# Kernel tuning notes

Hardware: AMD Instinct MI355X
Metric: run time of the kernel (lower is better)

The kernel has to match this reference:

```python
import jax, jax.numpy as jnp
import numpy as np

B, FIN, H, W = 16, 256, 32, 32
NH, FH = 8, 64
CIN = FIN + 2  # fin + 2 coordinate-grid pos channels
COUT = NH * FH


def setup_inputs() -> dict:
    key = jax.random.key(0)
    ks = jax.random.split(key, 9)
    s = 1.0 / np.sqrt(CIN)
    so = 1.0 / np.sqrt(COUT)
    return {
        "x": jax.random.normal(ks[0], (B, FIN, H, W), dtype=jnp.float32),
        "wq": jax.random.uniform(ks[1], (COUT, CIN), jnp.float32, -s, s),
        "bq": jax.random.uniform(ks[2], (COUT,), jnp.float32, -s, s),
        "wk": jax.random.uniform(ks[3], (COUT, CIN), jnp.float32, -s, s),
        "bk": jax.random.uniform(ks[4], (COUT,), jnp.float32, -s, s),
        "wv": jax.random.uniform(ks[5], (COUT, CIN), jnp.float32, -s, s),
        "bv": jax.random.uniform(ks[6], (COUT,), jnp.float32, -s, s),
        "wo": jax.random.uniform(ks[7], (FIN, COUT), jnp.float32, -so, so),
        "bo": jax.random.uniform(ks[8], (FIN,), jnp.float32, -so, so),
    }


def reference(x, wq, bq, wk, bk, wv, bv, wo, bo):
    b, c, h, w = x.shape
    n = h * w
    # PosEncoding: concat one linspace(-1,1) coordinate channel per spatial dim
    gy, gx = jnp.meshgrid(jnp.linspace(-1.0, 1.0, h), jnp.linspace(-1.0, 1.0, w), indexing="ij")
    pos = jnp.broadcast_to(jnp.stack([gy, gx])[None], (b, 2, h, w)).astype(x.dtype)
    t = jnp.concatenate([x, pos], axis=1).reshape(b, c + 2, n)  # [B, C+2, N]
    # 1x1 convs are per-token GEMMs
    q = (jnp.einsum("oc,bcn->bon", wq, t) + bq[:, None]).reshape(b, NH, FH, n)
    k = (jnp.einsum("oc,bcn->bon", wk, t) + bk[:, None]).reshape(b, NH, FH, n)
    v = (jnp.einsum("oc,bcn->bon", wv, t) + bv[:, None]).reshape(b, NH, FH, n)
    temp = FH ** 0.5
    attn = jax.nn.softmax(jnp.einsum("bhdn,bhdm->bhnm", q, k) / temp, axis=-1)
    o = jnp.einsum("bhnm,bhdm->bhdn", attn, v).reshape(b, NH * FH, n)
    o = jnp.einsum("oc,bcn->bon", wo, o) + bo[:, None]
    return x + o.reshape(b, c, h, w)
```

## Files before the change

kernel.cpp:

```cpp
#include <hip/hip_runtime.h>


typedef unsigned short u16;
typedef unsigned int   u32;
typedef __attribute__((ext_vector_type(8))) short  short8;
typedef __attribute__((ext_vector_type(4))) float  float4_;

#define MFMA16(a, b, c) __builtin_amdgcn_mfma_f32_16x16x32_bf16(a, b, c, 0, 0, 0)

__device__ __forceinline__ float bf2f(u16 u) {
    union { u32 i; float f; } v; v.i = ((u32)u) << 16; return v.f;
}
__device__ __forceinline__ u16 f2bf(float f) {
    union { float f; u32 i; } v; v.f = f;
    u32 r = v.i + 0x7FFFu + ((v.i >> 16) & 1u);
    return (u16)(r >> 16);
}
__device__ __forceinline__ u16 f2bf_fast(float f) {
    union { float f; u32 i; } v; v.f = f;
    return (u16)((v.i + 0x8000u) >> 16);
}

__global__ __launch_bounds__(256) void prep(
    const float* __restrict__ wq, const float* __restrict__ wk,
    const float* __restrict__ wv, const float* __restrict__ x,
    u16* __restrict__ wb, u16* __restrict__ xT)
{
    __shared__ float Lt[64][65];
    const int bid = blockIdx.x;
    const int tid = threadIdx.x;
    if (bid < 512) {
        int i = bid * 256 + tid;
        int o = i >> 8, c = i & 255;
        size_t si = (size_t)o * 258 + c;
        wb[i]          = f2bf(wq[si]);
        wb[131072 + i] = f2bf(wk[si]);
        wb[262144 + i] = f2bf(wv[si]);
    } else {
        int r = bid - 512;
        int n0 = (r & 15) * 64, c0 = ((r >> 4) & 3) * 64, b = r >> 6;
#pragma unroll
        for (int p = 0; p < 4; ++p) {
            int c = p * 16 + (tid >> 4);
            int nn = (tid & 15) * 4;
            float4 v = *(const float4*)&x[((size_t)(b * 256) + c0 + c) * 1024 + n0 + nn];
            Lt[c][nn + 0] = v.x; Lt[c][nn + 1] = v.y;
            Lt[c][nn + 2] = v.z; Lt[c][nn + 3] = v.w;
        }
        __syncthreads();
#pragma unroll
        for (int p = 0; p < 4; ++p) {
            int n = p * 16 + (tid >> 4);
            int cc = (tid & 15) * 4;
            ushort4 st;
            st.x = f2bf(Lt[cc + 0][n]); st.y = f2bf(Lt[cc + 1][n]);
            st.z = f2bf(Lt[cc + 2][n]); st.w = f2bf(Lt[cc + 3][n]);
            *(ushort4*)&xT[((size_t)(b << 10) + n0 + n) * 256 + c0 + cc] = st;
        }
    }
}

__global__ __launch_bounds__(256) void qkv_mfma(
    const u16* __restrict__ xT, const u16* __restrict__ wb,
    const float* __restrict__ wq, const float* __restrict__ wk,
    const float* __restrict__ wv,
    const float* __restrict__ bq, const float* __restrict__ bk,
    const float* __restrict__ bv,
    u16* __restrict__ qkvbuf)
{
    __shared__ u16 Wl[128][40];
    __shared__ u16 Tl[128][40];
    const int tid = threadIdx.x;
    const int lane = tid & 63, w = tid >> 6;
    const int quad = lane >> 4, m15 = lane & 15;
    const int n0 = blockIdx.x * 128, mt = blockIdx.y, b = blockIdx.z;
    const int mat = mt >> 2;
    const int m0 = mt * 128;
    const float* worig = (mat == 0) ? wq : ((mat == 1) ? wk : wv);
    const float* bias  = (mat == 0) ? bq : ((mat == 1) ? bk : bv);
    const float oscale = (mat == 1) ? 0.125f : 1.0f;
    u16* outbuf = qkvbuf + (size_t)mat * 8388608;

    float4_ acc[2][8];
#pragma unroll
    for (int s = 0; s < 2; ++s)
#pragma unroll
        for (int t = 0; t < 8; ++t) acc[s][t] = (float4_){0, 0, 0, 0};

    const int row = tid >> 2, col8 = (tid & 3) * 8;

    for (int cc0 = 0; cc0 < 256; cc0 += 32) {
        __syncthreads();
#pragma unroll
        for (int rr = 0; rr < 128; rr += 64) {
            *(short8*)&Wl[row + rr][col8] =
                *(const short8*)(wb + (size_t)(m0 + row + rr) * 256 + cc0 + col8);
            *(short8*)&Tl[row + rr][col8] =
                *(const short8*)(xT + ((size_t)(b << 10) + n0 + row + rr) * 256 + cc0 + col8);
        }
        __syncthreads();
        short8 af[2];
#pragma unroll
        for (int s = 0; s < 2; ++s)
            af[s] = *(const short8*)&Wl[w * 32 + s * 16 + m15][quad * 8];
#pragma unroll
        for (int t = 0; t < 8; ++t) {
            short8 bf = *(const short8*)&Tl[t * 16 + m15][quad * 8];
#pragma unroll
            for (int s = 0; s < 2; ++s)
                acc[s][t] = MFMA16(af[s], bf, acc[s][t]);
        }
    }

#pragma unroll
    for (int s = 0; s < 2; ++s) {
        float wg[4], wx[4], bi[4];
#pragma unroll
        for (int r = 0; r < 4; ++r) {
            int om = (mt & 3) * 128 + w * 32 + s * 16 + quad * 4 + r;
            wg[r] = worig[(size_t)om * 258 + 256];
            wx[r] = worig[(size_t)om * 258 + 257];
            bi[r] = bias[om];
        }
        const int h = (mt & 3) * 2 + ((w * 32 + s * 16) >> 6);
        const int dbase = ((w * 32 + s * 16) & 63) + quad * 4;
#pragma unroll
        for (int t = 0; t < 8; ++t) {
            int n = n0 + t * 16 + m15;
            float gy = -1.0f + 2.0f * (float)(n >> 5) / 31.0f;
            float gx = -1.0f + 2.0f * (float)(n & 31) / 31.0f;
            float v[4];
#pragma unroll
            for (int r = 0; r < 4; ++r)
                v[r] = (acc[s][t][r] + wg[r] * gy + wx[r] * gx + bi[r]) * oscale;
            if (mat != 2) {
                ushort4 st;
                st.x = f2bf(v[0]); st.y = f2bf(v[1]);
                st.z = f2bf(v[2]); st.w = f2bf(v[3]);
                *(ushort4*)&outbuf[((size_t)(b * 8 + h) * 1024 + n) * 64 + dbase] = st;
            } else {
#pragma unroll
                for (int r = 0; r < 4; ++r)
                    outbuf[((size_t)(b * 8 + h) * 64 + dbase + r) * 1024 + n] = f2bf(v[r]);
            }
        }
    }
}

__global__ __launch_bounds__(256) void attn_mfma(
    u16* __restrict__ qbuf, const u16* __restrict__ kbuf,
    const u16* __restrict__ vbuf)
{
    __shared__ u16 Kl[64][72];
    __shared__ u16 Vl[64][72];
    __shared__ u16 Pl[4][64][72];

    const int tid = threadIdx.x;
    const int lane = tid & 63, w = tid >> 6;
    const int quad = lane >> 4, m15 = lane & 15;
    const int q0 = blockIdx.y * 256;
    const int bh = blockIdx.x;
    u16* qb = qbuf + (size_t)bh * 65536;
    const u16* kb = kbuf + (size_t)bh * 65536;
    const u16* vb = vbuf + (size_t)bh * 65536;

    short8 qf[4][2];
#pragma unroll
    for (int s = 0; s < 4; ++s) {
        const u16* qr = qb + (size_t)(q0 + w * 64 + s * 16 + m15) * 64 + quad * 8;
        qf[s][0] = *(const short8*)qr;
        qf[s][1] = *(const short8*)(qr + 32);
    }

    float4_ O[4][4];
    float lp[4][4];
#pragma unroll
    for (int s = 0; s < 4; ++s)
#pragma unroll
        for (int t = 0; t < 4; ++t) { O[s][t] = (float4_){0,0,0,0}; lp[s][t] = 0.0f; }

    const int row = tid >> 3, c8 = (tid & 7) * 8;

    for (int kt0 = 0; kt0 < 1024; kt0 += 64) {
        __syncthreads();
#pragma unroll
        for (int rr = 0; rr < 64; rr += 32) {
            *(short8*)&Kl[row + rr][c8] =
                *(const short8*)(kb + (size_t)(kt0 + row + rr) * 64 + c8);
            *(short8*)&Vl[row + rr][c8] =
                *(const short8*)(vb + (size_t)(row + rr) * 1024 + kt0 + c8);
        }
        __syncthreads();

        float4_ S[4][4];
#pragma unroll
        for (int s = 0; s < 4; ++s)
#pragma unroll
            for (int t = 0; t < 4; ++t) S[s][t] = (float4_){0, 0, 0, 0};
#pragma unroll
        for (int c = 0; c < 2; ++c) {
            short8 bk[4];
#pragma unroll
            for (int t = 0; t < 4; ++t)
                bk[t] = *(const short8*)&Kl[t * 16 + m15][c * 32 + quad * 8];
#pragma unroll
            for (int s = 0; s < 4; ++s)
#pragma unroll
                for (int t = 0; t < 4; ++t)
                    S[s][t] = MFMA16(qf[s][c], bk[t], S[s][t]);
        }

#pragma unroll
        for (int s = 0; s < 4; ++s)
#pragma unroll
            for (int r = 0; r < 4; ++r) {
                float p0 = __expf(S[s][0][r]);
                float p1 = __expf(S[s][1][r]);
                float p2 = __expf(S[s][2][r]);
                float p3 = __expf(S[s][3][r]);
                u16* pr = &Pl[w][s * 16 + quad * 4 + r][m15];
                pr[0]  = f2bf_fast(p0);
                pr[16] = f2bf_fast(p1);
                pr[32] = f2bf_fast(p2);
                pr[48] = f2bf_fast(p3);
                lp[s][r] += (p0 + p1) + (p2 + p3);
            }

#pragma unroll
        for (int c = 0; c < 2; ++c) {
            short8 av[4];
#pragma unroll
            for (int dt = 0; dt < 4; ++dt)
                av[dt] = *(const short8*)&Vl[dt * 16 + m15][c * 32 + quad * 8];
#pragma unroll
            for (int s = 0; s < 4; ++s) {
                short8 bp = *(const short8*)&Pl[w][s * 16 + m15][c * 32 + quad * 8];
#pragma unroll
                for (int dt = 0; dt < 4; ++dt)
                    O[s][dt] = MFMA16(av[dt], bp, O[s][dt]);
            }
        }
    }

#pragma unroll
    for (int s = 0; s < 4; ++s)
#pragma unroll
        for (int r = 0; r < 4; ++r) {
            float v = lp[s][r];
            v += __shfl_xor(v, 1);
            v += __shfl_xor(v, 2);
            v += __shfl_xor(v, 4);
            v += __shfl_xor(v, 8);
            lp[s][r] = v;
        }

#pragma unroll
    for (int s = 0; s < 4; ++s) {
        int src = (m15 >> 2) * 16;
        float a0 = __shfl(lp[s][0], src);
        float a1 = __shfl(lp[s][1], src);
        float a2 = __shfl(lp[s][2], src);
        float a3 = __shfl(lp[s][3], src);
        int rr2 = m15 & 3;
        float lq = (rr2 & 2) ? ((rr2 & 1) ? a3 : a2) : ((rr2 & 1) ? a1 : a0);
        float linv = 1.0f / lq;
        int n = q0 + w * 64 + s * 16 + m15;
#pragma unroll
        for (int dt = 0; dt < 4; ++dt) {
            ushort4 st;
            st.x = f2bf(O[s][dt][0] * linv);
            st.y = f2bf(O[s][dt][1] * linv);
            st.z = f2bf(O[s][dt][2] * linv);
            st.w = f2bf(O[s][dt][3] * linv);
            *(ushort4*)&qb[(size_t)n * 64 + dt * 16 + quad * 4] = st;
        }
    }
}

__global__ __launch_bounds__(256) void proj_mfma(
    const u16* __restrict__ ao, const float* __restrict__ wo,
    const float* __restrict__ bo, const float* __restrict__ x,
    float* __restrict__ out)
{
    __shared__ u16 Wl[64][72];
    __shared__ u16 Tl[64][72];
    const int tid = threadIdx.x;
    const int lane = tid & 63, w = tid >> 6;
    const int quad = lane >> 4, m15 = lane & 15;
    const int n0 = blockIdx.x * 64, f0 = blockIdx.y * 64, b = blockIdx.z;

    float4_ acc[4] = {{0,0,0,0},{0,0,0,0},{0,0,0,0},{0,0,0,0}};
    const int row = tid >> 3, c8 = (tid & 7) * 8;

    for (int cc0 = 0; cc0 < 512; cc0 += 64) {
        __syncthreads();
        const int h = cc0 >> 6;
#pragma unroll
        for (int rr = 0; rr < 64; rr += 32) {
            const float* wsrc = wo + (size_t)(f0 + row + rr) * 512 + cc0 + c8;
            float4 v0 = *(const float4*)wsrc;
            float4 v1 = *(const float4*)(wsrc + 4);
            ushort4 s0, s1;
            s0.x = f2bf(v0.x); s0.y = f2bf(v0.y); s0.z = f2bf(v0.z); s0.w = f2bf(v0.w);
            s1.x = f2bf(v1.x); s1.y = f2bf(v1.y); s1.z = f2bf(v1.z); s1.w = f2bf(v1.w);
            *(ushort4*)&Wl[row + rr][c8]     = s0;
            *(ushort4*)&Wl[row + rr][c8 + 4] = s1;
            *(short8*)&Tl[row + rr][c8] =
                *(const short8*)(ao + ((size_t)((b << 3) + h) * 1024 + n0 + row + rr) * 64 + c8);
        }
        __syncthreads();
#pragma unroll
        for (int c = 0; c < 2; ++c) {
            short8 af = *(const short8*)&Wl[w * 16 + m15][c * 32 + quad * 8];
#pragma unroll
            for (int t = 0; t < 4; ++t) {
                short8 bf = *(const short8*)&Tl[t * 16 + m15][c * 32 + quad * 8];
                acc[t] = MFMA16(af, bf, acc[t]);
            }
        }
    }

    float bi[4];
#pragma unroll
    for (int r = 0; r < 4; ++r) bi[r] = bo[f0 + w * 16 + quad * 4 + r];
#pragma unroll
    for (int t = 0; t < 4; ++t) {
        int n = n0 + t * 16 + m15;
#pragma unroll
        for (int r = 0; r < 4; ++r) {
            int f = f0 + w * 16 + quad * 4 + r;
            size_t idx = ((size_t)(b * 256) + f) * 1024 + n;
            out[idx] = acc[t][r] + bi[r] + x[idx];
        }
    }
}

extern "C" void kernel_launch(void* const* d_in, const int* in_sizes, int n_in,
                              void* d_out, int out_size, void* d_ws, size_t ws_size,
                              hipStream_t stream) {
    const float* x  = (const float*)d_in[0];
    const float* wq = (const float*)d_in[1];
    const float* bq = (const float*)d_in[2];
    const float* wk = (const float*)d_in[3];
    const float* bk = (const float*)d_in[4];
    const float* wv = (const float*)d_in[5];
    const float* bv = (const float*)d_in[6];
    const float* wo = (const float*)d_in[7];
    const float* bo = (const float*)d_in[8];

    u16* qkvbuf = (u16*)d_ws;
    u16* region = qkvbuf + 3 * 8388608;
    u16* xT = region;
    u16* wb = region + 4194304;

    prep<<<1536, 256, 0, stream>>>(wq, wk, wv, x, wb, xT);

    qkv_mfma<<<dim3(8, 12, 16), 256, 0, stream>>>(
        xT, wb, wq, wk, wv, bq, bk, bv, qkvbuf);

    attn_mfma<<<dim3(128, 4), 256, 0, stream>>>(
        qkvbuf, qkvbuf + 8388608, qkvbuf + 16777216);

    proj_mfma<<<dim3(16, 4, 16), 256, 0, stream>>>(
        qkvbuf, wo, bo, x, (float*)d_out);
}
```

Measured before the change: 202.6 us.

## Load K/V MFMA fragments directly from global memory, drop LDS staging and barriers

The attention kernel no longer stages K and V tiles through shared memory with two block-wide barriers per key tile. Each wave loads its MFMA K and V fragments straight from global memory, relying on L2/L1 since all four waves read the same data. The K scale is folded with log2(e) so exp2f can replace __expf. The trade is redundant global loads per wave and possibly more exposed latency, in exchange for no barriers and less LDS use.

```diff
diff --git a/kernel.cpp b/kernel.cpp
--- a/kernel.cpp
+++ b/kernel.cpp
@@ -78,7 +78,7 @@
     const int m0 = mt * 128;
     const float* worig = (mat == 0) ? wq : ((mat == 1) ? wk : wv);
     const float* bias  = (mat == 0) ? bq : ((mat == 1) ? bk : bv);
-    const float oscale = (mat == 1) ? 0.125f : 1.0f;
+    const float oscale = (mat == 1) ? 0.18033688f : 1.0f;
     u16* outbuf = qkvbuf + (size_t)mat * 8388608;
 
     float4_ acc[2][8];
@@ -151,8 +151,6 @@
     u16* __restrict__ qbuf, const u16* __restrict__ kbuf,
     const u16* __restrict__ vbuf)
 {
-    __shared__ u16 Kl[64][72];
-    __shared__ u16 Vl[64][72];
     __shared__ u16 Pl[4][64][72];
 
     const int tid = threadIdx.x;
@@ -179,18 +177,16 @@
 #pragma unroll
         for (int t = 0; t < 4; ++t) { O[s][t] = (float4_){0,0,0,0}; lp[s][t] = 0.0f; }
 
-    const int row = tid >> 3, c8 = (tid & 7) * 8;
+    const u16* kfb = kb + (size_t)m15 * 64 + quad * 8;
+    const u16* vfb = vb + (size_t)m15 * 1024 + quad * 8;
 
     for (int kt0 = 0; kt0 < 1024; kt0 += 64) {
-        __syncthreads();
-#pragma unroll
-        for (int rr = 0; rr < 64; rr += 32) {
-            *(short8*)&Kl[row + rr][c8] =
-                *(const short8*)(kb + (size_t)(kt0 + row + rr) * 64 + c8);
-            *(short8*)&Vl[row + rr][c8] =
-                *(const short8*)(vb + (size_t)(row + rr) * 1024 + kt0 + c8);
-        }
-        __syncthreads();
+        short8 kf[2][4];
+#pragma unroll
+        for (int c = 0; c < 2; ++c)
+#pragma unroll
+            for (int t = 0; t < 4; ++t)
+                kf[c][t] = *(const short8*)(kfb + (size_t)(kt0 + t * 16) * 64 + c * 32);
 
         float4_ S[4][4];
 #pragma unroll
@@ -198,26 +194,28 @@
 #pragma unroll
             for (int t = 0; t < 4; ++t) S[s][t] = (float4_){0, 0, 0, 0};
 #pragma unroll
-        for (int c = 0; c < 2; ++c) {
-            short8 bk[4];
-#pragma unroll
-            for (int t = 0; t < 4; ++t)
-                bk[t] = *(const short8*)&Kl[t * 16 + m15][c * 32 + quad * 8];
+        for (int c = 0; c < 2; ++c)
 #pragma unroll
             for (int s = 0; s < 4; ++s)
 #pragma unroll
                 for (int t = 0; t < 4; ++t)
-                    S[s][t] = MFMA16(qf[s][c], bk[t], S[s][t]);
-        }
+                    S[s][t] = MFMA16(qf[s][c], kf[c][t], S[s][t]);
+
+        short8 vf[2][4];
+#pragma unroll
+        for (int c = 0; c < 2; ++c)
+#pragma unroll
+            for (int dt = 0; dt < 4; ++dt)
+                vf[c][dt] = *(const short8*)(vfb + (size_t)(dt * 16) * 1024 + kt0 + c * 32);
 
 #pragma unroll
         for (int s = 0; s < 4; ++s)
 #pragma unroll
             for (int r = 0; r < 4; ++r) {
-                float p0 = __expf(S[s][0][r]);
-                float p1 = __expf(S[s][1][r]);
-                float p2 = __expf(S[s][2][r]);
-                float p3 = __expf(S[s][3][r]);
+                float p0 = exp2f(S[s][0][r]);
+                float p1 = exp2f(S[s][1][r]);
+                float p2 = exp2f(S[s][2][r]);
+                float p3 = exp2f(S[s][3][r]);
                 u16* pr = &Pl[w][s * 16 + quad * 4 + r][m15];
                 pr[0]  = f2bf_fast(p0);
                 pr[16] = f2bf_fast(p1);
@@ -227,19 +225,14 @@
             }
 
 #pragma unroll
-        for (int c = 0; c < 2; ++c) {
-            short8 av[4];
-#pragma unroll
-            for (int dt = 0; dt < 4; ++dt)
-                av[dt] = *(const short8*)&Vl[dt * 16 + m15][c * 32 + quad * 8];
+        for (int c = 0; c < 2; ++c)
 #pragma unroll
             for (int s = 0; s < 4; ++s) {
                 short8 bp = *(const short8*)&Pl[w][s * 16 + m15][c * 32 + quad * 8];
 #pragma unroll
                 for (int dt = 0; dt < 4; ++dt)
-                    O[s][dt] = MFMA16(av[dt], bp, O[s][dt]);
+                    O[s][dt] = MFMA16(vf[c][dt], bp, O[s][dt]);
             }
-        }
     }
 
 #pragma unroll
```

Result: slower. 237.1 us (+17.0%).

## Double-buffer K/V tiles in attention, shrink QKV tiles, fold log2e into exp2

Applied to the files above, without the earlier changes.

The attention kernel now double-buffers its K/V shared-memory tiles. The next tile is prefetched into registers while the current one is computed, which removes one barrier per iteration and hides global load latency. The QKV projection kernel moves from 128x128 tiles with a 32-deep k-step to 64x64 tiles with a 64-deep k-step over a 4x larger grid, trading reuse for more blocks and parallelism. The K scale now includes log2(e) so the softmax can use exp2f instead of __expf. This doubles K/V LDS use in attention and reduces per-block operand reuse in the projection.

```diff
diff --git a/kernel.cpp b/kernel.cpp
--- a/kernel.cpp
+++ b/kernel.cpp
@@ -68,80 +68,78 @@
     const float* __restrict__ bv,
     u16* __restrict__ qkvbuf)
 {
-    __shared__ u16 Wl[128][40];
-    __shared__ u16 Tl[128][40];
+    __shared__ u16 Wl[64][72];
+    __shared__ u16 Tl[64][72];
     const int tid = threadIdx.x;
     const int lane = tid & 63, w = tid >> 6;
     const int quad = lane >> 4, m15 = lane & 15;
-    const int n0 = blockIdx.x * 128, mt = blockIdx.y, b = blockIdx.z;
-    const int mat = mt >> 2;
-    const int m0 = mt * 128;
+    const int n0 = blockIdx.x * 64, by = blockIdx.y, b = blockIdx.z;
+    const int mat = by >> 3, h = by & 7;
     const float* worig = (mat == 0) ? wq : ((mat == 1) ? wk : wv);
     const float* bias  = (mat == 0) ? bq : ((mat == 1) ? bk : bv);
-    const float oscale = (mat == 1) ? 0.125f : 1.0f;
+    const float oscale = (mat == 1) ? 0.18033688f : 1.0f;
+    const int wrow0 = mat * 512 + h * 64;
     u16* outbuf = qkvbuf + (size_t)mat * 8388608;
 
-    float4_ acc[2][8];
-#pragma unroll
-    for (int s = 0; s < 2; ++s)
-#pragma unroll
-        for (int t = 0; t < 8; ++t) acc[s][t] = (float4_){0, 0, 0, 0};
-
-    const int row = tid >> 2, col8 = (tid & 3) * 8;
-
-    for (int cc0 = 0; cc0 < 256; cc0 += 32) {
-        __syncthreads();
-#pragma unroll
-        for (int rr = 0; rr < 128; rr += 64) {
-            *(short8*)&Wl[row + rr][col8] =
-                *(const short8*)(wb + (size_t)(m0 + row + rr) * 256 + cc0 + col8);
-            *(short8*)&Tl[row + rr][col8] =
-                *(const short8*)(xT + ((size_t)(b << 10) + n0 + row + rr) * 256 + cc0 + col8);
-        }
-        __syncthreads();
-        short8 af[2];
-#pragma unroll
-        for (int s = 0; s < 2; ++s)
-            af[s] = *(const short8*)&Wl[w * 32 + s * 16 + m15][quad * 8];
-#pragma unroll
-        for (int t = 0; t < 8; ++t) {
-            short8 bf = *(const short8*)&Tl[t * 16 + m15][quad * 8];
-#pragma unroll
-            for (int s = 0; s < 2; ++s)
-                acc[s][t] = MFMA16(af[s], bf, acc[s][t]);
-        }
-    }
-
-#pragma unroll
-    for (int s = 0; s < 2; ++s) {
-        float wg[4], wx[4], bi[4];
-#pragma unroll
-        for (int r = 0; r < 4; ++r) {
-            int om = (mt & 3) * 128 + w * 32 + s * 16 + quad * 4 + r;
-            wg[r] = worig[(size_t)om * 258 + 256];
-            wx[r] = worig[(size_t)om * 258 + 257];
-            bi[r] = bias[om];
-        }
-        const int h = (mt & 3) * 2 + ((w * 32 + s * 16) >> 6);
-        const int dbase = ((w * 32 + s * 16) & 63) + quad * 4;
-#pragma unroll
-        for (int t = 0; t < 8; ++t) {
+    float4_ acc[4] = {{0,0,0,0},{0,0,0,0},{0,0,0,0},{0,0,0,0}};
+    const int row = tid >> 3, c8 = (tid & 7) * 8;
+
+    for (int cc0 = 0; cc0 < 256; cc0 += 64) {
+        __syncthreads();
+#pragma unroll
+        for (int rr = 0; rr < 64; rr += 32) {
+            *(short8*)&Wl[row + rr][c8] =
+                *(const short8*)(wb + (size_t)(wrow0 + row + rr) * 256 + cc0 + c8);
+            *(short8*)&Tl[row + rr][c8] =
+                *(const short8*)(xT + ((size_t)(b << 10) + n0 + row + rr) * 256 + cc0 + c8);
+        }
+        __syncthreads();
+#pragma unroll
+        for (int c = 0; c < 2; ++c) {
+            short8 af = *(const short8*)&Wl[w * 16 + m15][c * 32 + quad * 8];
+#pragma unroll
+            for (int t = 0; t < 4; ++t) {
+                short8 bf = *(const short8*)&Tl[t * 16 + m15][c * 32 + quad * 8];
+                acc[t] = MFMA16(af, bf, acc[t]);
+            }
+        }
+    }
+
+    float wg[4], wx[4], bi[4];
+#pragma unroll
+    for (int r = 0; r < 4; ++r) {
+        int o = h * 64 + w * 16 + quad * 4 + r;
+        wg[r] = worig[(size_t)o * 258 + 256];
+        wx[r] = worig[(size_t)o * 258 + 257];
+        bi[r] = bias[o];
+    }
+#pragma unroll
+    for (int t = 0; t < 4; ++t) {
+        int n = n0 + t * 16 + m15;
+        float gy = -1.0f + 2.0f * (float)(n >> 5) / 31.0f;
+        float gx = -1.0f + 2.0f * (float)(n & 31) / 31.0f;
+#pragma unroll
+        for (int r = 0; r < 4; ++r)
+            acc[t][r] = (acc[t][r] + wg[r] * gy + wx[r] * gx + bi[r]) * oscale;
+    }
+
+    if (mat != 2) {
+#pragma unroll
+        for (int t = 0; t < 4; ++t) {
             int n = n0 + t * 16 + m15;
-            float gy = -1.0f + 2.0f * (float)(n >> 5) / 31.0f;
-            float gx = -1.0f + 2.0f * (float)(n & 31) / 31.0f;
-            float v[4];
-#pragma unroll
-            for (int r = 0; r < 4; ++r)
-                v[r] = (acc[s][t][r] + wg[r] * gy + wx[r] * gx + bi[r]) * oscale;
-            if (mat != 2) {
-                ushort4 st;
-                st.x = f2bf(v[0]); st.y = f2bf(v[1]);
-                st.z = f2bf(v[2]); st.w = f2bf(v[3]);
-                *(ushort4*)&outbuf[((size_t)(b * 8 + h) * 1024 + n) * 64 + dbase] = st;
-            } else {
-#pragma unroll
-                for (int r = 0; r < 4; ++r)
-                    outbuf[((size_t)(b * 8 + h) * 64 + dbase + r) * 1024 + n] = f2bf(v[r]);
+            ushort4 st;
+            st.x = f2bf(acc[t][0]); st.y = f2bf(acc[t][1]);
+            st.z = f2bf(acc[t][2]); st.w = f2bf(acc[t][3]);
+            *(ushort4*)&outbuf[((size_t)(b * 8 + h) * 1024 + n) * 64 + w * 16 + quad * 4] = st;
+        }
+    } else {
+#pragma unroll
+        for (int t = 0; t < 4; ++t) {
+            int n = n0 + t * 16 + m15;
+#pragma unroll
+            for (int r = 0; r < 4; ++r) {
+                int d = w * 16 + quad * 4 + r;
+                outbuf[((size_t)(b * 8 + h) * 64 + d) * 1024 + n] = f2bf(acc[t][r]);
             }
         }
     }
@@ -151,8 +149,8 @@
     u16* __restrict__ qbuf, const u16* __restrict__ kbuf,
     const u16* __restrict__ vbuf)
 {
-    __shared__ u16 Kl[64][72];
-    __shared__ u16 Vl[64][72];
+    __shared__ u16 Kl[2][64][72];
+    __shared__ u16 Vl[2][64][72];
     __shared__ u16 Pl[4][64][72];
 
     const int tid = threadIdx.x;
@@ -181,16 +179,30 @@
 
     const int row = tid >> 3, c8 = (tid & 7) * 8;
 
-    for (int kt0 = 0; kt0 < 1024; kt0 += 64) {
-        __syncthreads();
-#pragma unroll
-        for (int rr = 0; rr < 64; rr += 32) {
-            *(short8*)&Kl[row + rr][c8] =
-                *(const short8*)(kb + (size_t)(kt0 + row + rr) * 64 + c8);
-            *(short8*)&Vl[row + rr][c8] =
-                *(const short8*)(vb + (size_t)(row + rr) * 1024 + kt0 + c8);
-        }
-        __syncthreads();
+    short8 kpre[2], vpre[2];
+#pragma unroll
+    for (int i = 0; i < 2; ++i) {
+        kpre[i] = *(const short8*)(kb + (size_t)(row + i * 32) * 64 + c8);
+        vpre[i] = *(const short8*)(vb + (size_t)(row + i * 32) * 1024 + c8);
+    }
+#pragma unroll
+    for (int i = 0; i < 2; ++i) {
+        *(short8*)&Kl[0][row + i * 32][c8] = kpre[i];
+        *(short8*)&Vl[0][row + i * 32][c8] = vpre[i];
+    }
+    __syncthreads();
+
+    for (int it = 0; it < 16; ++it) {
+        const int p = it & 1;
+        const int kt0 = it * 64;
+
+        if (it < 15) {
+#pragma unroll
+            for (int i = 0; i < 2; ++i) {
+                kpre[i] = *(const short8*)(kb + (size_t)(kt0 + 64 + row + i * 32) * 64 + c8);
+                vpre[i] = *(const short8*)(vb + (size_t)(row + i * 32) * 1024 + kt0 + 64 + c8);
+            }
+        }
 
         float4_ S[4][4];
 #pragma unroll
@@ -202,7 +214,7 @@
             short8 bk[4];
 #pragma unroll
             for (int t = 0; t < 4; ++t)
-                bk[t] = *(const short8*)&Kl[t * 16 + m15][c * 32 + quad * 8];
+                bk[t] = *(const short8*)&Kl[p][t * 16 + m15][c * 32 + quad * 8];
 #pragma unroll
             for (int s = 0; s < 4; ++s)
 #pragma unroll
@@ -214,10 +226,10 @@
         for (int s = 0; s < 4; ++s)
 #pragma unroll
             for (int r = 0; r < 4; ++r) {
-                float p0 = __expf(S[s][0][r]);
-                float p1 = __expf(S[s][1][r]);
-                float p2 = __expf(S[s][2][r]);
-                float p3 = __expf(S[s][3][r]);
+                float p0 = exp2f(S[s][0][r]);
+                float p1 = exp2f(S[s][1][r]);
+                float p2 = exp2f(S[s][2][r]);
+                float p3 = exp2f(S[s][3][r]);
                 u16* pr = &Pl[w][s * 16 + quad * 4 + r][m15];
                 pr[0]  = f2bf_fast(p0);
                 pr[16] = f2bf_fast(p1);
@@ -231,7 +243,7 @@
             short8 av[4];
 #pragma unroll
             for (int dt = 0; dt < 4; ++dt)
-                av[dt] = *(const short8*)&Vl[dt * 16 + m15][c * 32 + quad * 8];
+                av[dt] = *(const short8*)&Vl[p][dt * 16 + m15][c * 32 + quad * 8];
 #pragma unroll
             for (int s = 0; s < 4; ++s) {
                 short8 bp = *(const short8*)&Pl[w][s * 16 + m15][c * 32 + quad * 8];
@@ -239,6 +251,15 @@
                 for (int dt = 0; dt < 4; ++dt)
                     O[s][dt] = MFMA16(av[dt], bp, O[s][dt]);
             }
+        }
+
+        if (it < 15) {
+#pragma unroll
+            for (int i = 0; i < 2; ++i) {
+                *(short8*)&Kl[p ^ 1][row + i * 32][c8] = kpre[i];
+                *(short8*)&Vl[p ^ 1][row + i * 32][c8] = vpre[i];
+            }
+            __syncthreads();
         }
     }
 
@@ -355,7 +376,7 @@
 
     prep<<<1536, 256, 0, stream>>>(wq, wk, wv, x, wb, xT);
 
-    qkv_mfma<<<dim3(8, 12, 16), 256, 0, stream>>>(
+    qkv_mfma<<<dim3(16, 24, 16), 256, 0, stream>>>(
         xT, wb, wq, wk, wv, bq, bk, bv, qkvbuf);
 
     attn_mfma<<<dim3(128, 4), 256, 0, stream>>>(
```

Result: slower. 238.0 us (+17.5%).
